# Kernel optimization log

Measured on AMD Instinct MI355X. Metric: run time of the kernel, lower is better.

## Reference

```python
import jax, jax.numpy as jnp
import numpy as np

NUM_CLASSES = 5  # sleep stages: W, N1, N2, N3, REM
N = 4194304


def setup_inputs() -> dict:
    key = jax.random.key(0)
    k1, k2 = jax.random.split(key)
    inputs = jax.random.normal(k1, (N, NUM_CLASSES), dtype=jnp.float32)
    targets = jax.random.randint(k2, (N,), 0, NUM_CLASSES, dtype=jnp.int32)
    return {"inputs": inputs, "targets": targets}


def reference(inputs, targets):
    # Mean False Error loss: per-class mean of per-sample cross-entropy,
    # summed over classes that are present in the batch.
    # per-sample CE loss (stable log-softmax, single pass)
    logp = jax.nn.log_softmax(inputs, axis=-1)                    # [N, C]
    per_sample = -jnp.take_along_axis(logp, targets[:, None].astype(jnp.int32), axis=1)[:, 0]  # [N]
    # segment-reduce by class label (replaces the python grouping loop)
    loss_sums = jax.ops.segment_sum(per_sample, targets, num_segments=NUM_CLASSES)             # [C]
    counts = jax.ops.segment_sum(jnp.ones_like(per_sample), targets, num_segments=NUM_CLASSES) # [C]
    # per-class mean; empty classes contribute 0
    means = jnp.where(counts > 0, loss_sums / jnp.maximum(counts, 1.0), 0.0)
    return jnp.sum(means)
```

## Files before the change

kernel.cpp:

```cpp
#include <hip/hip_runtime.h>

#define NCLS 5
#define NSAMP 4194304
#define BLOCK 256
#define GRID 2048
#define NTHREADS (GRID * BLOCK)
#define NVALS (2 * NCLS)

__device__ __forceinline__ void accum_sample(float l0, float l1, float l2, float l3, float l4,
                                             int t, float sums[NCLS], unsigned int& packed_cnt) {
    float s = __expf(l0) + __expf(l1) + __expf(l2) + __expf(l3) + __expf(l4);
    float lt = (t == 0) ? l0 : (t == 1) ? l1 : (t == 2) ? l2 : (t == 3) ? l3 : l4;
    float ce = __logf(s) - lt;
#pragma unroll
    for (int k = 0; k < NCLS; ++k) {
        sums[k] += (t == k) ? ce : 0.0f;
    }
    packed_cnt += 1u << (6 * t);
}

__device__ __forceinline__ void block_reduce_10(float sums[NCLS], float cnts[NCLS],
                                                float* result10) {
#pragma unroll
    for (int k = 0; k < NCLS; ++k) {
#pragma unroll
        for (int off = 32; off > 0; off >>= 1) {
            sums[k] += __shfl_down(sums[k], off, 64);
            cnts[k] += __shfl_down(cnts[k], off, 64);
        }
    }
    __shared__ float ls[BLOCK / 64][NVALS];
    const int lane = threadIdx.x & 63;
    const int wave = threadIdx.x >> 6;
    if (lane == 0) {
#pragma unroll
        for (int k = 0; k < NCLS; ++k) {
            ls[wave][k] = sums[k];
            ls[wave][NCLS + k] = cnts[k];
        }
    }
    __syncthreads();
    if (threadIdx.x < NVALS) {
        float v = 0.f;
#pragma unroll
        for (int w = 0; w < BLOCK / 64; ++w) v += ls[w][threadIdx.x];
        *result10 = v;
    }
}

__global__ __launch_bounds__(BLOCK) void mfe_fused(const float* __restrict__ inputs,
                                                   const int* __restrict__ targets,
                                                   float* __restrict__ partial ,
                                                   unsigned int* __restrict__ flags ,
                                                   float* __restrict__ out) {
    const int tid = blockIdx.x * BLOCK + threadIdx.x;

    const int base0 = tid * 4;
    const int base1 = (NTHREADS + tid) * 4;
    const float4* p0 = (const float4*)(inputs + (size_t)base0 * NCLS);
    const float4* p1 = (const float4*)(inputs + (size_t)base1 * NCLS);
    float4 a0 = p0[0], b0 = p0[1], c0 = p0[2], d0 = p0[3], e0 = p0[4];
    float4 a1 = p1[0], b1 = p1[1], c1 = p1[2], d1 = p1[3], e1 = p1[4];
    int4 t0 = *(const int4*)(targets + base0);
    int4 t1 = *(const int4*)(targets + base1);

    float sums[NCLS] = {0.f, 0.f, 0.f, 0.f, 0.f};
    unsigned int packed = 0;

    accum_sample(a0.x, a0.y, a0.z, a0.w, b0.x, t0.x, sums, packed);
    accum_sample(b0.y, b0.z, b0.w, c0.x, c0.y, t0.y, sums, packed);
    accum_sample(c0.z, c0.w, d0.x, d0.y, d0.z, t0.z, sums, packed);
    accum_sample(d0.w, e0.x, e0.y, e0.z, e0.w, t0.w, sums, packed);
    accum_sample(a1.x, a1.y, a1.z, a1.w, b1.x, t1.x, sums, packed);
    accum_sample(b1.y, b1.z, b1.w, c1.x, c1.y, t1.y, sums, packed);
    accum_sample(c1.z, c1.w, d1.x, d1.y, d1.z, t1.z, sums, packed);
    accum_sample(d1.w, e1.x, e1.y, e1.z, e1.w, t1.w, sums, packed);

    float cnts[NCLS];
#pragma unroll
    for (int k = 0; k < NCLS; ++k) {
        cnts[k] = (float)((packed >> (6 * k)) & 63u);
    }

    float total;
    block_reduce_10(sums, cnts, &total);

    if (threadIdx.x < NVALS) {
        __hip_atomic_store(&partial[threadIdx.x * GRID + blockIdx.x], total,
                           __ATOMIC_RELAXED, __HIP_MEMORY_SCOPE_AGENT);
    }
    asm volatile("s_waitcnt vmcnt(0)" ::: "memory");
    if (threadIdx.x == 0) {
        __hip_atomic_store(&flags[blockIdx.x], 1u,
                           __ATOMIC_RELAXED, __HIP_MEMORY_SCOPE_AGENT);
    }

    if (blockIdx.x != 0) return;

#pragma unroll 1
    for (int i = threadIdx.x; i < GRID; i += BLOCK) {
        while (__hip_atomic_load(&flags[i], __ATOMIC_RELAXED,
                                 __HIP_MEMORY_SCOPE_AGENT) == 0u) {
            __builtin_amdgcn_s_sleep(2);
        }
    }
    __syncthreads();
    asm volatile("" ::: "memory");

    float fsums[NCLS], fcnts[NCLS];
#pragma unroll
    for (int k = 0; k < NCLS; ++k) {
        float s = 0.f, c = 0.f;
#pragma unroll
        for (int i = 0; i < GRID / BLOCK; ++i) {
            s += __hip_atomic_load(&partial[k * GRID + threadIdx.x + i * BLOCK],
                                   __ATOMIC_RELAXED, __HIP_MEMORY_SCOPE_AGENT);
            c += __hip_atomic_load(&partial[(NCLS + k) * GRID + threadIdx.x + i * BLOCK],
                                   __ATOMIC_RELAXED, __HIP_MEMORY_SCOPE_AGENT);
        }
        fsums[k] = s;
        fcnts[k] = c;
    }

    float ftot;
    block_reduce_10(fsums, fcnts, &ftot);

    __shared__ float fin[NVALS];
    if (threadIdx.x < NVALS) fin[threadIdx.x] = ftot;
    __syncthreads();
    if (threadIdx.x == 0) {
        float loss = 0.f;
#pragma unroll
        for (int k = 0; k < NCLS; ++k) {
            float cnt = fin[NCLS + k];
            if (cnt > 0.f) loss += fin[k] / cnt;
        }
        out[0] = loss;
    }
}

extern "C" void kernel_launch(void* const* d_in, const int* in_sizes, int n_in,
                              void* d_out, int out_size, void* d_ws, size_t ws_size,
                              hipStream_t stream) {
    const float* inputs = (const float*)d_in[0];
    const int* targets = (const int*)d_in[1];
    float* out = (float*)d_out;
    float* partial = (float*)d_ws;
    unsigned int* flags =
        (unsigned int*)((char*)d_ws + (size_t)NVALS * GRID * sizeof(float));

    hipMemsetAsync(flags, 0, GRID * sizeof(unsigned int), stream);
    mfe_fused<<<GRID, BLOCK, 0, stream>>>(inputs, targets, partial, flags, out);
}
```

Measured before the change: 136.8 us.

## Stage input tiles through LDS with direct global-to-LDS swizzled loads

Each block now loads a contiguous chunk of 1024 samples straight into shared memory with global_load_lds, so every wave's loads are fully coalesced. The LDS index is XOR-swizzled to avoid bank conflicts when each thread then reads its five float4s. The grid doubles to 4096 blocks and each thread handles 4 samples instead of 8. The cost is an extra LDS round trip, a block barrier, and a larger partial/flag array for the single-block final reduction.

```diff
diff --git a/kernel.cpp b/kernel.cpp
--- a/kernel.cpp
+++ b/kernel.cpp
@@ -3,8 +3,9 @@
 #define NCLS 5
 #define NSAMP 4194304
 #define BLOCK 256
-#define GRID 2048
-#define NTHREADS (GRID * BLOCK)
+#define GRID 4096
+#define SAMP_PER_BLOCK (NSAMP / GRID)
+#define CHUNK_F4 (SAMP_PER_BLOCK * NCLS / 4)
 #define NVALS (2 * NCLS)
 
 __device__ __forceinline__ void accum_sample(float l0, float l1, float l2, float l3, float l4,
@@ -48,33 +49,48 @@
     }
 }
 
+__device__ __forceinline__ int swz(int F) { return F ^ ((F >> 3) & 7); }
+
+__device__ __forceinline__ void gload_lds16(const float4* g, float4* l) {
+    __builtin_amdgcn_global_load_lds(
+        (__attribute__((address_space(1))) const void*)g,
+        (__attribute__((address_space(3))) void*)l, 16, 0, 0);
+}
+
 __global__ __launch_bounds__(BLOCK) void mfe_fused(const float* __restrict__ inputs,
                                                    const int* __restrict__ targets,
                                                    float* __restrict__ partial ,
                                                    unsigned int* __restrict__ flags ,
                                                    float* __restrict__ out) {
-    const int tid = blockIdx.x * BLOCK + threadIdx.x;
+    const int T = threadIdx.x;
+    const int b = blockIdx.x;
+    const int w = T >> 6;
+    const int lane = T & 63;
+    const size_t samp0 = (size_t)b * SAMP_PER_BLOCK;
+    const float4* gin = (const float4*)(inputs + samp0 * NCLS);
 
-    const int base0 = tid * 4;
-    const int base1 = (NTHREADS + tid) * 4;
-    const float4* p0 = (const float4*)(inputs + (size_t)base0 * NCLS);
-    const float4* p1 = (const float4*)(inputs + (size_t)base1 * NCLS);
-    float4 a0 = p0[0], b0 = p0[1], c0 = p0[2], d0 = p0[3], e0 = p0[4];
-    float4 a1 = p1[0], b1 = p1[1], c1 = p1[2], d1 = p1[3], e1 = p1[4];
-    int4 t0 = *(const int4*)(targets + base0);
-    int4 t1 = *(const int4*)(targets + base1);
+    __shared__ float4 lds[CHUNK_F4];
+
+    int4 tg = *(const int4*)(targets + samp0 + 4 * T);
+
+#pragma unroll
+    for (int j = 0; j < 5; ++j) {
+        const int base = 320 * w + 64 * j;
+        gload_lds16(gin + swz(base + lane), &lds[base]);
+    }
+    asm volatile("s_waitcnt vmcnt(0)" ::: "memory");
+    __syncthreads();
+
+    float4 r[5];
+#pragma unroll
+    for (int k = 0; k < 5; ++k) r[k] = lds[swz(5 * T + k)];
 
     float sums[NCLS] = {0.f, 0.f, 0.f, 0.f, 0.f};
     unsigned int packed = 0;
-
-    accum_sample(a0.x, a0.y, a0.z, a0.w, b0.x, t0.x, sums, packed);
-    accum_sample(b0.y, b0.z, b0.w, c0.x, c0.y, t0.y, sums, packed);
-    accum_sample(c0.z, c0.w, d0.x, d0.y, d0.z, t0.z, sums, packed);
-    accum_sample(d0.w, e0.x, e0.y, e0.z, e0.w, t0.w, sums, packed);
-    accum_sample(a1.x, a1.y, a1.z, a1.w, b1.x, t1.x, sums, packed);
-    accum_sample(b1.y, b1.z, b1.w, c1.x, c1.y, t1.y, sums, packed);
-    accum_sample(c1.z, c1.w, d1.x, d1.y, d1.z, t1.z, sums, packed);
-    accum_sample(d1.w, e1.x, e1.y, e1.z, e1.w, t1.w, sums, packed);
+    accum_sample(r[0].x, r[0].y, r[0].z, r[0].w, r[1].x, tg.x, sums, packed);
+    accum_sample(r[1].y, r[1].z, r[1].w, r[2].x, r[2].y, tg.y, sums, packed);
+    accum_sample(r[2].z, r[2].w, r[3].x, r[3].y, r[3].z, tg.z, sums, packed);
+    accum_sample(r[3].w, r[4].x, r[4].y, r[4].z, r[4].w, tg.w, sums, packed);
 
     float cnts[NCLS];
 #pragma unroll
```

Measured after the change: 142.1 us. +3.9%, slower.
